# Kernel optimization log

Hardware: AMD Instinct MI355X
Metric: run time of the kernel (lower is better)

Reference implementation:

```python
import jax, jax.numpy as jnp
import numpy as np

N_NODES = 100000
N_GRAPHS = 64
IN_CH, HID, OUT = 128, 64, 2
N_EDGES = 1600000


def gcn_conv(x, row, col, W, b):
    # PyG GCNConv: h = x @ W; add self-loops; symmetric normalization
    # deg[i] = 1 (self-loop) + in-degree at target nodes (col)
    N = x.shape[0]
    h = x @ W                                            # [N, F_out]
    deg = jnp.ones((N,), h.dtype).at[col].add(1.0)       # [N]
    dinv = jax.lax.rsqrt(deg)                            # deg^{-1/2}
    coef = dinv[row] * dinv[col]                         # [E] edge norm
    msg = h[row] * coef[:, None]                         # gather + scale
    agg = jnp.zeros_like(h).at[col].add(msg)             # scatter-add at targets
    agg = agg + h * (dinv * dinv)[:, None]               # self-loop term
    return agg + b


def setup_inputs() -> dict:
    key = jax.random.key(0)
    k1, k2, k3, k4, k5, k6, k7 = jax.random.split(key, 7)
    x = jax.random.normal(k1, (N_NODES, IN_CH), jnp.float32)
    edge_index = jax.random.randint(k2, (2, N_EDGES), 0, N_NODES, jnp.int64)
    batch = jnp.sort(jax.random.randint(k3, (N_NODES,), 0, N_GRAPHS, jnp.int64))
    s = 1.0 / np.sqrt(IN_CH)
    W1 = jax.random.uniform(k4, (IN_CH, HID), jnp.float32, -s, s)
    b1 = jnp.zeros((HID,), jnp.float32)
    sh = 1.0 / np.sqrt(HID)
    W2 = jax.random.uniform(k5, (HID, HID), jnp.float32, -sh, sh)
    b2 = jnp.zeros((HID,), jnp.float32)
    W3 = jax.random.uniform(k6, (HID, HID), jnp.float32, -sh, sh)
    b3 = jnp.zeros((HID,), jnp.float32)
    Wlin = jax.random.uniform(k7, (HID, OUT), jnp.float32, -sh, sh)
    blin = jnp.zeros((OUT,), jnp.float32)
    return {"x": x, "edge_index": edge_index, "batch": batch,
            "W1": W1, "b1": b1, "W2": W2, "b2": b2, "W3": W3, "b3": b3,
            "Wlin": Wlin, "blin": blin}


def reference(x, edge_index, batch, W1, b1, W2, b2, W3, b3, Wlin, blin):
    row, col = edge_index[0], edge_index[1]
    h = gcn_conv(x, row, col, W1, b1)
    h = jax.nn.relu(h)
    h = gcn_conv(h, row, col, W2, b2)
    h = jax.nn.relu(h)
    h = gcn_conv(h, row, col, W3, b3)    # no relu after last conv
    # global_mean_pool over batch ids
    pooled = jax.ops.segment_sum(h, batch, num_segments=N_GRAPHS)
    counts = jax.ops.segment_sum(jnp.ones((h.shape[0],), h.dtype), batch,
                                 num_segments=N_GRAPHS)
    pooled = pooled / jnp.maximum(counts, 1.0)[:, None]
    # dropout p=0.5 is identity in eval mode
    return pooled @ Wlin + blin          # [N_GRAPHS, OUT]
```

## Files before the change

kernel.cpp:

```cpp
#include <hip/hip_runtime.h>
#include <hip/hip_fp16.h>

#define IN_CH 128
#define HIDDEN 64

typedef _Float16 half8 __attribute__((ext_vector_type(8)));
typedef float f32x4 __attribute__((ext_vector_type(4)));


__global__ __launch_bounds__(512)
void bucket_hist_kernel(const int* __restrict__ col, int* __restrict__ bhist, int E) {
    __shared__ int h[512];
    h[threadIdx.x] = 0;
    __syncthreads();
    const int start = blockIdx.x * 8192;
    const int end = min(start + 8192, E);
    for (int e = start + threadIdx.x; e < end; e += 512)
        atomicAdd(&h[col[e] >> 8], 1);
    __syncthreads();
    if (h[threadIdx.x]) atomicAdd(&bhist[threadIdx.x], h[threadIdx.x]);
}

__global__ __launch_bounds__(512)
void bucket_scan_kernel(const int* __restrict__ bhist, int* __restrict__ bbase,
                        int* __restrict__ bpos, int* __restrict__ off,
                        int nb, int N, int E) {
    __shared__ int s[512];
    const int t = threadIdx.x;
    const int v = (t < nb) ? bhist[t] : 0;
    s[t] = v;
    __syncthreads();
    for (int d = 1; d < 512; d <<= 1) {
        int u = (t >= d) ? s[t - d] : 0;
        __syncthreads();
        s[t] += u;
        __syncthreads();
    }
    const int b = s[t] - v;
    if (t < nb) { bbase[t] = b; bpos[t] = b; }
    if (t == 0) { bbase[nb] = E; off[N] = E; }
}

__global__ __launch_bounds__(512)
void bucket_scatter_kernel(const int* __restrict__ row, const int* __restrict__ col,
                           int* __restrict__ bpos, unsigned* __restrict__ tmp, int E) {
    __shared__ int h[512];
    __shared__ int base[512];
    h[threadIdx.x] = 0;
    __syncthreads();
    const int start = blockIdx.x * 8192;
    const int end = min(start + 8192, E);
    for (int e = start + threadIdx.x; e < end; e += 512)
        atomicAdd(&h[col[e] >> 8], 1);
    __syncthreads();
    const int i = threadIdx.x;
    base[i] = h[i] ? atomicAdd(&bpos[i], h[i]) : 0;
    h[i] = 0;
    __syncthreads();
    for (int e = start + threadIdx.x; e < end; e += 512) {
        const int c = col[e];
        const int bk = c >> 8;
        const int p = base[bk] + atomicAdd(&h[bk], 1);
        tmp[p] = ((unsigned)row[e] << 8) | (unsigned)(c & 255);
    }
}

__global__ __launch_bounds__(256)
void bucket_sort_kernel(const unsigned* __restrict__ tmp, const int* __restrict__ bbase,
                        int* __restrict__ off, float* __restrict__ dinv,
                        int* __restrict__ srcrow, int N) {
    __shared__ int cnt[256];
    __shared__ int sc[256];
    const int b = blockIdx.x;
    const int node0 = b << 8;
    const int t = threadIdx.x;
    const int lo = bbase[b], hi = bbase[b + 1];
    cnt[t] = 0;
    __syncthreads();
    for (int j = lo + t; j < hi; j += 256)
        atomicAdd(&cnt[tmp[j] & 255u], 1);
    __syncthreads();
    const int v = cnt[t];
    sc[t] = v;
    __syncthreads();
    for (int d = 1; d < 256; d <<= 1) {
        int u = (t >= d) ? sc[t - d] : 0;
        __syncthreads();
        sc[t] += u;
        __syncthreads();
    }
    const int excl = sc[t] - v;
    const int node = node0 + t;
    if (node < N) {
        off[node] = lo + excl;
        dinv[node] = rsqrtf((float)v + 1.0f);
    }
    cnt[t] = lo + excl;
    __syncthreads();
    for (int j = lo + t; j < hi; j += 256) {
        const unsigned pk = tmp[j];
        const int p = atomicAdd(&cnt[pk & 255u], 1);
        srcrow[p] = (int)(pk >> 8);
    }
}


__global__ void pack_kernel(const float* __restrict__ W, _Float16* __restrict__ Wp, int K) {
    const int tid = threadIdx.x;
    const int l = tid & 63;
    const int g = tid >> 6;
    const int kb = (l >> 4) * 8;
    const int c = 16 * g + (l & 15);
    for (int s = 0; s < K / 32; ++s) {
        half8 v;
#pragma unroll
        for (int j = 0; j < 8; ++j)
            v[j] = (_Float16)W[(size_t)(32 * s + kb + j) * 64 + c];
        *reinterpret_cast<half8*>(&Wp[((size_t)(s * 4 + g) * 64 + l) * 8]) = v;
    }
}


template <int K, bool AF32>
__global__ __launch_bounds__(256)
void gemm_mfma_kernel(const void* __restrict__ Aptr, const _Float16* __restrict__ Wp,
                      const float* __restrict__ dinv, _Float16* __restrict__ Hs, int N) {
    const int tid = threadIdx.x;
    const int l = tid & 63;
    const int w = tid >> 6;
    const int r0 = blockIdx.x * 64 + w * 16;
    const int arow_ = r0 + (l & 15);
    const int arow = arow_ < N ? arow_ : N - 1;
    const int kb = (l >> 4) * 8;

    f32x4 acc[4] = {};
#pragma unroll
    for (int s = 0; s < K / 32; ++s) {
        half8 a;
        if constexpr (AF32) {
            const float* A = (const float*)Aptr;
            const float4 f0 = *reinterpret_cast<const float4*>(&A[(size_t)arow * K + 32 * s + kb]);
            const float4 f1 = *reinterpret_cast<const float4*>(&A[(size_t)arow * K + 32 * s + kb + 4]);
            a[0] = (_Float16)f0.x; a[1] = (_Float16)f0.y;
            a[2] = (_Float16)f0.z; a[3] = (_Float16)f0.w;
            a[4] = (_Float16)f1.x; a[5] = (_Float16)f1.y;
            a[6] = (_Float16)f1.z; a[7] = (_Float16)f1.w;
        } else {
            const _Float16* A = (const _Float16*)Aptr;
            a = *reinterpret_cast<const half8*>(&A[(size_t)arow * K + 32 * s + kb]);
        }
        const half8* Wb = reinterpret_cast<const half8*>(&Wp[(size_t)(s * 4) * 64 * 8]);
#pragma unroll
        for (int g = 0; g < 4; ++g) {
            const half8 b = Wb[g * 64 + l];
            acc[g] = __builtin_amdgcn_mfma_f32_16x16x32_f16(a, b, acc[g], 0, 0, 0);
        }
    }

    const int rb = r0 + (l >> 4) * 4;
    float dv[4];
#pragma unroll
    for (int j = 0; j < 4; ++j) {
        const int r = rb + j;
        dv[j] = dinv[r < N ? r : N - 1];
    }
#pragma unroll
    for (int g = 0; g < 4; ++g) {
#pragma unroll
        for (int j = 0; j < 4; ++j) {
            const int r = rb + j;
            if (r < N)
                Hs[(size_t)r * 64 + g * 16 + (l & 15)] = (_Float16)(acc[g][j] * dv[j]);
        }
    }
}


template <bool RELU>
__global__ __launch_bounds__(256)
void gather_kernel(const __half* __restrict__ Hs, const float* __restrict__ dinv,
                   const int* __restrict__ off, const int* __restrict__ srcrow,
                   const float* __restrict__ bias, __half* __restrict__ A, int N) {
    const int tid  = threadIdx.x;
    const int lane = tid & 63;
    const int q    = lane >> 4;
    const int fl   = (lane & 15) << 2;
    const int wid  = tid >> 6;
    const int c    = blockIdx.x * 16 + wid * 4 + q;
    const int cc   = (c < N) ? c : N - 1;
    const int lo = off[cc], hi = off[cc + 1];

    float4 acc = make_float4(0.f, 0.f, 0.f, 0.f);
    int j = lo;
    while (__any(j < hi)) {
        int idx[8];
#pragma unroll
        for (int u = 0; u < 8; ++u) {
            const int jj = j + u;
            idx[u] = srcrow[jj < hi ? jj : (hi > lo ? hi - 1 : 0)];
        }
        uint2 hv[8];
#pragma unroll
        for (int u = 0; u < 8; ++u)
            hv[u] = *reinterpret_cast<const uint2*>(&Hs[(size_t)idx[u] * 64 + fl]);
#pragma unroll
        for (int u = 0; u < 8; ++u) {
            if (j + u < hi) {
                union { uint2 uu; __half2 h2[2]; } v; v.uu = hv[u];
                const float2 a = __half22float2(v.h2[0]);
                const float2 b = __half22float2(v.h2[1]);
                acc.x += a.x; acc.y += a.y; acc.z += b.x; acc.w += b.y;
            }
        }
        j += 8;
    }

    if (c < N) {
        const float dc = dinv[c];
        union { uint2 uu; __half2 h2[2]; } sv;
        sv.uu = *reinterpret_cast<const uint2*>(&Hs[(size_t)c * 64 + fl]);
        const float2 s0 = __half22float2(sv.h2[0]);
        const float2 s1 = __half22float2(sv.h2[1]);
        const float4 bl = *reinterpret_cast<const float4*>(&bias[fl]);
        float4 o;
        o.x = dc * (acc.x + s0.x) + bl.x;
        o.y = dc * (acc.y + s0.y) + bl.y;
        o.z = dc * (acc.z + s1.x) + bl.z;
        o.w = dc * (acc.w + s1.y) + bl.w;
        if (RELU) {
            o.x = fmaxf(o.x, 0.f); o.y = fmaxf(o.y, 0.f);
            o.z = fmaxf(o.z, 0.f); o.w = fmaxf(o.w, 0.f);
        }
        union { uint2 uu; __half2 h2[2]; } ov;
        ov.h2[0] = __floats2half2_rn(o.x, o.y);
        ov.h2[1] = __floats2half2_rn(o.z, o.w);
        *reinterpret_cast<uint2*>(&A[(size_t)c * 64 + fl]) = ov.uu;
    }
}


__global__ __launch_bounds__(256)
void pool_kernel(const __half* __restrict__ A, const int* __restrict__ batch,
                 float* __restrict__ pooled, int* __restrict__ gcnt, int N) {
    const int g = blockIdx.x >> 3;
    const int stripe = blockIdx.x & 7;
    int lo = 0, hi = N;
    while (lo < hi) { int m = (lo + hi) >> 1; if (batch[m] < g) lo = m + 1; else hi = m; }
    const int beg = lo;
    lo = beg; hi = N;
    while (lo < hi) { int m = (lo + hi) >> 1; if (batch[m] < g + 1) lo = m + 1; else hi = m; }
    const int end = lo;

    const int lane = threadIdx.x & 63;
    const int wsid = stripe * 4 + (threadIdx.x >> 6);
    float acc = 0.f;
    for (int i = beg + wsid; i < end; i += 32)
        acc += __half2float(A[(size_t)i * 64 + lane]);
    atomicAdd(&pooled[g * 64 + lane], acc);
    if (stripe == 0 && threadIdx.x == 0) gcnt[g] = end - beg;
}

__global__ void final_kernel(const float* __restrict__ pooled, const int* __restrict__ gcnt,
                             const float* __restrict__ Wlin, const float* __restrict__ blin,
                             float* __restrict__ out) {
    const int t = threadIdx.x;
    const int g = t >> 1, o = t & 1;
    const float c = (float)max(gcnt[g], 1);
    float acc = 0.f;
    for (int k = 0; k < 64; ++k)
        acc = fmaf(pooled[g * 64 + k], Wlin[k * 2 + o], acc);
    out[g * 2 + o] = acc / c + blin[o];
}


extern "C" void kernel_launch(void* const* d_in, const int* in_sizes, int n_in,
                              void* d_out, int out_size, void* d_ws, size_t ws_size,
                              hipStream_t stream) {
    const float* x     = (const float*)d_in[0];
    const int*   ei    = (const int*)d_in[1];
    const int*   batch = (const int*)d_in[2];
    const float* W1    = (const float*)d_in[3];
    const float* b1    = (const float*)d_in[4];
    const float* W2    = (const float*)d_in[5];
    const float* b2    = (const float*)d_in[6];
    const float* W3    = (const float*)d_in[7];
    const float* b3    = (const float*)d_in[8];
    const float* Wlin  = (const float*)d_in[9];
    const float* blin  = (const float*)d_in[10];

    const int N = in_sizes[0] / IN_CH;
    const int E = in_sizes[1] / 2;
    const int* row = ei;
    const int* col = ei + E;
    const int nb = (N + 255) >> 8;

    char* p = (char*)d_ws;
    auto alloc = [&](size_t bytes) {
        char* q = p;
        p += (bytes + 511) & ~(size_t)511;
        return q;
    };
    int*      off    = (int*)alloc((size_t)(N + 1) * 4);
    float*    dinv   = (float*)alloc((size_t)N * 4);
    int*      srcrow = (int*)alloc((size_t)E * 4);
    unsigned* tmp    = (unsigned*)alloc((size_t)E * 4);
    _Float16* Hbuf   = (_Float16*)alloc((size_t)N * HIDDEN * 2);
    _Float16* Abuf   = (_Float16*)alloc((size_t)N * HIDDEN * 2);
    _Float16* Wp1    = (_Float16*)alloc((size_t)IN_CH * 64 * 2);
    _Float16* Wp2    = (_Float16*)alloc((size_t)HIDDEN * 64 * 2);
    _Float16* Wp3    = (_Float16*)alloc((size_t)HIDDEN * 64 * 2);
    int*      bhist  = (int*)alloc(512 * 4);
    int*      bbase  = (int*)alloc(513 * 4);
    int*      bpos   = (int*)alloc(512 * 4);
    float*    pooled = (float*)alloc(64 * 64 * 4);
    int*      gcnt   = (int*)alloc(64 * 4);
    (void)ws_size; (void)n_in; (void)out_size;

    hipMemsetAsync(bhist, 0, 512 * 4, stream);
    const int eb = (E + 8191) / 8192;
    bucket_hist_kernel<<<eb, 512, 0, stream>>>(col, bhist, E);
    bucket_scan_kernel<<<1, 512, 0, stream>>>(bhist, bbase, bpos, off, nb, N, E);
    bucket_scatter_kernel<<<eb, 512, 0, stream>>>(row, col, bpos, tmp, E);
    bucket_sort_kernel<<<nb, 256, 0, stream>>>(tmp, bbase, off, dinv, srcrow, N);

    pack_kernel<<<1, 256, 0, stream>>>(W1, Wp1, IN_CH);
    pack_kernel<<<1, 256, 0, stream>>>(W2, Wp2, HIDDEN);
    pack_kernel<<<1, 256, 0, stream>>>(W3, Wp3, HIDDEN);

    const int gemm_grid   = (N + 63) / 64;
    const int gather_grid = (N + 15) / 16;
    gemm_mfma_kernel<IN_CH, true><<<gemm_grid, 256, 0, stream>>>(x, Wp1, dinv, Hbuf, N);
    gather_kernel<true><<<gather_grid, 256, 0, stream>>>((const __half*)Hbuf, dinv, off, srcrow, b1, (__half*)Abuf, N);
    gemm_mfma_kernel<HIDDEN, false><<<gemm_grid, 256, 0, stream>>>(Abuf, Wp2, dinv, Hbuf, N);
    gather_kernel<true><<<gather_grid, 256, 0, stream>>>((const __half*)Hbuf, dinv, off, srcrow, b2, (__half*)Abuf, N);
    gemm_mfma_kernel<HIDDEN, false><<<gemm_grid, 256, 0, stream>>>(Abuf, Wp3, dinv, Hbuf, N);
    gather_kernel<false><<<gather_grid, 256, 0, stream>>>((const __half*)Hbuf, dinv, off, srcrow, b3, (__half*)Abuf, N);

    hipMemsetAsync(pooled, 0, 64 * 64 * 4, stream);
    pool_kernel<<<512, 256, 0, stream>>>((const __half*)Abuf, batch, pooled, gcnt, N);
    final_kernel<<<1, 128, 0, stream>>>(pooled, gcnt, Wlin, blin, (float*)d_out);
}
```

Before: 314.0 us.

## Merge weight packing and memsets into kernels, shrink sort buckets to 128 nodes

Folds the three weight-pack launches into one three-block kernel that also zeroes the bucket histogram, and moves the pooled-buffer zeroing into the scan kernel, removing two memsets and two launches. The CSR bucket sort now uses 1024 buckets of 128 nodes with 1024-thread blocks, so the per-bucket sort kernel runs on more, smaller blocks. This relies on N/128 fitting in 1024 buckets (N=100000 gives 782) and on row indices fitting in 25 bits after the shift by 7.

```diff
diff --git a/kernel.cpp b/kernel.cpp
--- a/kernel.cpp
+++ b/kernel.cpp
@@ -3,110 +3,23 @@
 
 #define IN_CH 128
 #define HIDDEN 64
+#define NB 1024
 
 typedef _Float16 half8 __attribute__((ext_vector_type(8)));
 typedef float f32x4 __attribute__((ext_vector_type(4)));
 
 
-__global__ __launch_bounds__(512)
-void bucket_hist_kernel(const int* __restrict__ col, int* __restrict__ bhist, int E) {
-    __shared__ int h[512];
-    h[threadIdx.x] = 0;
-    __syncthreads();
-    const int start = blockIdx.x * 8192;
-    const int end = min(start + 8192, E);
-    for (int e = start + threadIdx.x; e < end; e += 512)
-        atomicAdd(&h[col[e] >> 8], 1);
-    __syncthreads();
-    if (h[threadIdx.x]) atomicAdd(&bhist[threadIdx.x], h[threadIdx.x]);
-}
-
-__global__ __launch_bounds__(512)
-void bucket_scan_kernel(const int* __restrict__ bhist, int* __restrict__ bbase,
-                        int* __restrict__ bpos, int* __restrict__ off,
-                        int nb, int N, int E) {
-    __shared__ int s[512];
-    const int t = threadIdx.x;
-    const int v = (t < nb) ? bhist[t] : 0;
-    s[t] = v;
-    __syncthreads();
-    for (int d = 1; d < 512; d <<= 1) {
-        int u = (t >= d) ? s[t - d] : 0;
-        __syncthreads();
-        s[t] += u;
-        __syncthreads();
-    }
-    const int b = s[t] - v;
-    if (t < nb) { bbase[t] = b; bpos[t] = b; }
-    if (t == 0) { bbase[nb] = E; off[N] = E; }
-}
-
-__global__ __launch_bounds__(512)
-void bucket_scatter_kernel(const int* __restrict__ row, const int* __restrict__ col,
-                           int* __restrict__ bpos, unsigned* __restrict__ tmp, int E) {
-    __shared__ int h[512];
-    __shared__ int base[512];
-    h[threadIdx.x] = 0;
-    __syncthreads();
-    const int start = blockIdx.x * 8192;
-    const int end = min(start + 8192, E);
-    for (int e = start + threadIdx.x; e < end; e += 512)
-        atomicAdd(&h[col[e] >> 8], 1);
-    __syncthreads();
-    const int i = threadIdx.x;
-    base[i] = h[i] ? atomicAdd(&bpos[i], h[i]) : 0;
-    h[i] = 0;
-    __syncthreads();
-    for (int e = start + threadIdx.x; e < end; e += 512) {
-        const int c = col[e];
-        const int bk = c >> 8;
-        const int p = base[bk] + atomicAdd(&h[bk], 1);
-        tmp[p] = ((unsigned)row[e] << 8) | (unsigned)(c & 255);
-    }
-}
-
-__global__ __launch_bounds__(256)
-void bucket_sort_kernel(const unsigned* __restrict__ tmp, const int* __restrict__ bbase,
-                        int* __restrict__ off, float* __restrict__ dinv,
-                        int* __restrict__ srcrow, int N) {
-    __shared__ int cnt[256];
-    __shared__ int sc[256];
-    const int b = blockIdx.x;
-    const int node0 = b << 8;
-    const int t = threadIdx.x;
-    const int lo = bbase[b], hi = bbase[b + 1];
-    cnt[t] = 0;
-    __syncthreads();
-    for (int j = lo + t; j < hi; j += 256)
-        atomicAdd(&cnt[tmp[j] & 255u], 1);
-    __syncthreads();
-    const int v = cnt[t];
-    sc[t] = v;
-    __syncthreads();
-    for (int d = 1; d < 256; d <<= 1) {
-        int u = (t >= d) ? sc[t - d] : 0;
-        __syncthreads();
-        sc[t] += u;
-        __syncthreads();
-    }
-    const int excl = sc[t] - v;
-    const int node = node0 + t;
-    if (node < N) {
-        off[node] = lo + excl;
-        dinv[node] = rsqrtf((float)v + 1.0f);
-    }
-    cnt[t] = lo + excl;
-    __syncthreads();
-    for (int j = lo + t; j < hi; j += 256) {
-        const unsigned pk = tmp[j];
-        const int p = atomicAdd(&cnt[pk & 255u], 1);
-        srcrow[p] = (int)(pk >> 8);
-    }
-}
-
-
-__global__ void pack_kernel(const float* __restrict__ W, _Float16* __restrict__ Wp, int K) {
+__global__ __launch_bounds__(256)
+void pack3_kernel(const float* __restrict__ W1, const float* __restrict__ W2,
+                  const float* __restrict__ W3, _Float16* __restrict__ Wp1,
+                  _Float16* __restrict__ Wp2, _Float16* __restrict__ Wp3,
+                  int* __restrict__ bhist) {
     const int tid = threadIdx.x;
+    if (blockIdx.x == 0)
+        for (int i = tid; i < NB; i += 256) bhist[i] = 0;
+    const float* W = (blockIdx.x == 0) ? W1 : (blockIdx.x == 1) ? W2 : W3;
+    _Float16* Wp   = (blockIdx.x == 0) ? Wp1 : (blockIdx.x == 1) ? Wp2 : Wp3;
+    const int K    = (blockIdx.x == 0) ? IN_CH : HIDDEN;
     const int l = tid & 63;
     const int g = tid >> 6;
     const int kb = (l >> 4) * 8;
@@ -117,6 +30,108 @@
         for (int j = 0; j < 8; ++j)
             v[j] = (_Float16)W[(size_t)(32 * s + kb + j) * 64 + c];
         *reinterpret_cast<half8*>(&Wp[((size_t)(s * 4 + g) * 64 + l) * 8]) = v;
+    }
+}
+
+
+__global__ __launch_bounds__(1024)
+void bucket_hist_kernel(const int* __restrict__ col, int* __restrict__ bhist, int E) {
+    __shared__ int h[NB];
+    h[threadIdx.x] = 0;
+    __syncthreads();
+    const int start = blockIdx.x * 8192;
+    const int end = min(start + 8192, E);
+    for (int e = start + threadIdx.x; e < end; e += 1024)
+        atomicAdd(&h[col[e] >> 7], 1);
+    __syncthreads();
+    if (h[threadIdx.x]) atomicAdd(&bhist[threadIdx.x], h[threadIdx.x]);
+}
+
+__global__ __launch_bounds__(1024)
+void bucket_scan_kernel(const int* __restrict__ bhist, int* __restrict__ bbase,
+                        int* __restrict__ bpos, int* __restrict__ off,
+                        float* __restrict__ pooled, int N, int E) {
+    __shared__ int s[NB];
+    const int t = threadIdx.x;
+    pooled[t] = 0.f; pooled[t + 1024] = 0.f;
+    pooled[t + 2048] = 0.f; pooled[t + 3072] = 0.f;
+    const int v = bhist[t];
+    s[t] = v;
+    __syncthreads();
+    for (int d = 1; d < 1024; d <<= 1) {
+        int u = (t >= d) ? s[t - d] : 0;
+        __syncthreads();
+        s[t] += u;
+        __syncthreads();
+    }
+    const int b = s[t] - v;
+    bbase[t] = b;
+    bpos[t] = b;
+    if (t == 0) { bbase[NB] = E; off[N] = E; }
+}
+
+__global__ __launch_bounds__(1024)
+void bucket_scatter_kernel(const int* __restrict__ row, const int* __restrict__ col,
+                           int* __restrict__ bpos, unsigned* __restrict__ tmp, int E) {
+    __shared__ int h[NB];
+    __shared__ int base[NB];
+    h[threadIdx.x] = 0;
+    __syncthreads();
+    const int start = blockIdx.x * 8192;
+    const int end = min(start + 8192, E);
+    for (int e = start + threadIdx.x; e < end; e += 1024)
+        atomicAdd(&h[col[e] >> 7], 1);
+    __syncthreads();
+    const int i = threadIdx.x;
+    base[i] = h[i] ? atomicAdd(&bpos[i], h[i]) : 0;
+    h[i] = 0;
+    __syncthreads();
+    for (int e = start + threadIdx.x; e < end; e += 1024) {
+        const int c = col[e];
+        const int bk = c >> 7;
+        const int p = base[bk] + atomicAdd(&h[bk], 1);
+        tmp[p] = ((unsigned)row[e] << 7) | (unsigned)(c & 127);
+    }
+}
+
+__global__ __launch_bounds__(256)
+void bucket_sort_kernel(const unsigned* __restrict__ tmp, const int* __restrict__ bbase,
+                        int* __restrict__ off, float* __restrict__ dinv,
+                        int* __restrict__ srcrow, int N) {
+    __shared__ int cnt[128];
+    __shared__ int sc[128];
+    const int b = blockIdx.x;
+    const int node0 = b << 7;
+    const int t = threadIdx.x;
+    const int lo = bbase[b], hi = bbase[b + 1];
+    if (t < 128) cnt[t] = 0;
+    __syncthreads();
+    for (int j = lo + t; j < hi; j += 256)
+        atomicAdd(&cnt[tmp[j] & 127u], 1);
+    __syncthreads();
+    const int v = (t < 128) ? cnt[t] : 0;
+    if (t < 128) sc[t] = v;
+    __syncthreads();
+    for (int d = 1; d < 128; d <<= 1) {
+        int u = (t >= d && t < 128) ? sc[t - d] : 0;
+        __syncthreads();
+        if (t < 128) sc[t] += u;
+        __syncthreads();
+    }
+    if (t < 128) {
+        const int excl = sc[t] - v;
+        const int node = node0 + t;
+        if (node < N) {
+            off[node] = lo + excl;
+            dinv[node] = rsqrtf((float)v + 1.0f);
+        }
+        cnt[t] = lo + excl;
+    }
+    __syncthreads();
+    for (int j = lo + t; j < hi; j += 256) {
+        const unsigned pk = tmp[j];
+        const int p = atomicAdd(&cnt[pk & 127u], 1);
+        srcrow[p] = (int)(pk >> 7);
     }
 }
 
@@ -292,7 +307,7 @@
     const int E = in_sizes[1] / 2;
     const int* row = ei;
     const int* col = ei + E;
-    const int nb = (N + 255) >> 8;
+    const int nb = (N + 127) >> 7;
 
     char* p = (char*)d_ws;
     auto alloc = [&](size_t bytes) {
@@ -309,23 +324,20 @@
     _Float16* Wp1    = (_Float16*)alloc((size_t)IN_CH * 64 * 2);
     _Float16* Wp2    = (_Float16*)alloc((size_t)HIDDEN * 64 * 2);
     _Float16* Wp3    = (_Float16*)alloc((size_t)HIDDEN * 64 * 2);
-    int*      bhist  = (int*)alloc(512 * 4);
-    int*      bbase  = (int*)alloc(513 * 4);
-    int*      bpos   = (int*)alloc(512 * 4);
+    int*      bhist  = (int*)alloc(NB * 4);
+    int*      bbase  = (int*)alloc((NB + 1) * 4);
+    int*      bpos   = (int*)alloc(NB * 4);
     float*    pooled = (float*)alloc(64 * 64 * 4);
     int*      gcnt   = (int*)alloc(64 * 4);
     (void)ws_size; (void)n_in; (void)out_size;
 
-    hipMemsetAsync(bhist, 0, 512 * 4, stream);
+    pack3_kernel<<<3, 256, 0, stream>>>(W1, W2, W3, Wp1, Wp2, Wp3, bhist);
+
     const int eb = (E + 8191) / 8192;
-    bucket_hist_kernel<<<eb, 512, 0, stream>>>(col, bhist, E);
-    bucket_scan_kernel<<<1, 512, 0, stream>>>(bhist, bbase, bpos, off, nb, N, E);
-    bucket_scatter_kernel<<<eb, 512, 0, stream>>>(row, col, bpos, tmp, E);
+    bucket_hist_kernel<<<eb, 1024, 0, stream>>>(col, bhist, E);
+    bucket_scan_kernel<<<1, 1024, 0, stream>>>(bhist, bbase, bpos, off, pooled, N, E);
+    bucket_scatter_kernel<<<eb, 1024, 0, stream>>>(row, col, bpos, tmp, E);
     bucket_sort_kernel<<<nb, 256, 0, stream>>>(tmp, bbase, off, dinv, srcrow, N);
-
-    pack_kernel<<<1, 256, 0, stream>>>(W1, Wp1, IN_CH);
-    pack_kernel<<<1, 256, 0, stream>>>(W2, Wp2, HIDDEN);
-    pack_kernel<<<1, 256, 0, stream>>>(W3, Wp3, HIDDEN);
 
     const int gemm_grid   = (N + 63) / 64;
     const int gather_grid = (N + 15) / 16;
@@ -336,7 +348,6 @@
     gemm_mfma_kernel<HIDDEN, false><<<gemm_grid, 256, 0, stream>>>(Abuf, Wp3, dinv, Hbuf, N);
     gather_kernel<false><<<gather_grid, 256, 0, stream>>>((const __half*)Hbuf, dinv, off, srcrow, b3, (__half*)Abuf, N);
 
-    hipMemsetAsync(pooled, 0, 64 * 64 * 4, stream);
     pool_kernel<<<512, 256, 0, stream>>>((const __half*)Abuf, batch, pooled, gcnt, N);
     final_kernel<<<1, 128, 0, stream>>>(pooled, gcnt, Wlin, blin, (float*)d_out);
 }
```

After: 302.7 us. 3.6% less time.
